# Optimization experiments

Measured on AMD Instinct MI355X. Metric: run time of the kernel, lower is better.

## Reference

```python
import jax, jax.numpy as jnp
import numpy as np

HEADS = 16
GROUPS = 4


def setup_inputs() -> dict:
    key = jax.random.key(0)
    k1, k2, k3, k4 = jax.random.split(key, 4)
    d_model = 2048
    d_kv = d_model * GROUPS // HEADS  # 512
    x = jax.random.normal(k1, (2, 2048, d_model), dtype=jnp.float32)
    Wq = jax.random.normal(k2, (d_model, d_model), dtype=jnp.float32) * (d_model ** -0.5)
    Wk = jax.random.normal(k3, (d_kv, d_model), dtype=jnp.float32) * (d_model ** -0.5)
    Wv = jax.random.normal(k4, (d_kv, d_model), dtype=jnp.float32) * (d_model ** -0.5)
    return {"x": x, "Wq": Wq, "Wk": Wk, "Wv": Wv}


def reference(x, Wq, Wk, Wv):
    b, t, c = x.shape
    hd = c // HEADS  # head dim
    h2g = HEADS // GROUPS  # query heads per kv group
    # projections (nn.Linear applies x @ W.T)
    q = (x @ Wq.T).reshape(b, t, HEADS, hd).transpose(0, 2, 1, 3)   # [b,H,t,hd]
    k = (x @ Wk.T).reshape(b, t, GROUPS, hd).transpose(0, 2, 1, 3)  # [b,G,t,hd]
    v = (x @ Wv.T).reshape(b, t, GROUPS, hd).transpose(0, 2, 1, 3)  # [b,G,t,hd]
    # GQA broadcast: group query heads by kv group
    qg = q.reshape(b, GROUPS, h2g, t, hd)                            # [b,G,h2g,t,hd]
    scores = jnp.einsum('bghqd,bgkd->bghqk', qg, k) * (hd ** -0.5)  # [b,G,h2g,t,t]
    causal = jnp.tril(jnp.ones((t, t), dtype=bool))
    scores = jnp.where(causal, scores, -jnp.inf)
    weights = jax.nn.softmax(scores, axis=-1)
    out = jnp.einsum('bghqk,bgkd->bghqd', weights, v)               # [b,G,h2g,t,hd]
    out = out.reshape(b, HEADS, t, hd).transpose(0, 2, 1, 3).reshape(b, t, c)
    return out
```

## Files before the change

kernel.cpp:

```cpp
#include <hip/hip_runtime.h>
#include <hip/hip_bf16.h>

typedef __bf16 bf16x8 __attribute__((ext_vector_type(8)));
typedef float f32x4 __attribute__((ext_vector_type(4)));

#define MFMA16(a,b,c) __builtin_amdgcn_mfma_f32_16x16x32_bf16(a,b,c,0,0,0)
#define GLL16(src, dst) __builtin_amdgcn_global_load_lds( \
    (const __attribute__((address_space(1))) unsigned int*)(src), \
    (__attribute__((address_space(3))) unsigned int*)(dst), 16, 0, 0)
#define WAIT_VM(n)  asm volatile("s_waitcnt vmcnt(" #n ")")
#define BAR() __builtin_amdgcn_s_barrier()

__device__ inline unsigned int pack_bf16(float a, float b) {
    unsigned short ua = __builtin_bit_cast(unsigned short, (__bf16)a);
    unsigned short ub = __builtin_bit_cast(unsigned short, (__bf16)b);
    return ((unsigned int)ub << 16) | ua;
}
__device__ inline short bf_s(float v) {
    __bf16 b = (__bf16)v;
    return __builtin_bit_cast(short, b);
}

__global__ __launch_bounds__(256) void cvt_all(const float* __restrict__ x,
                                               const float* __restrict__ wq,
                                               const float* __restrict__ wk,
                                               const float* __restrict__ wv,
                                               __bf16* __restrict__ xb,
                                               __bf16* __restrict__ wb) {
    int bid = blockIdx.x;
    int rb = bid >> 4, ks = bid & 15;
    int t = threadIdx.x;
    int row = t & 15;
    int k8 = ks * 16 + (t >> 4);
    int k = k8 * 8;

    const float* src;
    __bf16* dptr;
    size_t tin = (size_t)(k8 >> 2) * 512 + (size_t)(k8 & 3) * 128 + row * 8;
    if (rb < 256) {
        src  = x + (size_t)(rb * 16 + row) * 2048 + k;
        dptr = xb + (size_t)rb * 32768 + tin;
    } else {
        int wr = (rb - 256) * 16 + row;
        if (wr < 2048)      src = wq + (size_t)wr * 2048 + k;
        else if (wr < 2560) src = wk + (size_t)(wr - 2048) * 2048 + k;
        else                src = wv + (size_t)(wr - 2560) * 2048 + k;
        dptr = wb + (size_t)(rb - 256) * 32768 + tin;
    }
    float4 a = *(const float4*)src;
    float4 b = *(const float4*)(src + 4);
    bf16x8 r;
    r[0] = (__bf16)a.x; r[1] = (__bf16)a.y; r[2] = (__bf16)a.z; r[3] = (__bf16)a.w;
    r[4] = (__bf16)b.x; r[5] = (__bf16)b.y; r[6] = (__bf16)b.z; r[7] = (__bf16)b.w;
    *(bf16x8*)dptr = r;
}

__global__ __launch_bounds__(512, 6) void gemm_qkv(const __bf16* __restrict__ A,
                                                   const __bf16* __restrict__ B,
                                                   __bf16* __restrict__ Qb,
                                                   __bf16* __restrict__ Kf,
                                                   __bf16* __restrict__ Vf,
                                                   float qscale) {
    __shared__ __bf16 As[2 * 4096];
    __shared__ __bf16 Bs[2 * 4096];

    int tid = threadIdx.x;
    int wave = tid >> 6, lane = tid & 63;
    int quad = lane >> 4, l16 = lane & 15;
    int wr = wave >> 1, wc = wave & 1;

    int tm = blockIdx.x & 31, tn = blockIdx.x >> 5;

    const __bf16* Atile = A + (size_t)(tm * 8 + wave) * 32768 + lane * 8;
    const __bf16* Btile = B + (size_t)(tn * 8 + wave) * 32768 + lane * 8;

    f32x4 acc[2][4] = {};

    auto stage = [&](int kb, int buf) {
        GLL16(Atile + (size_t)kb * 512, As + buf * 4096 + wave * 512 + lane * 8);
        GLL16(Btile + (size_t)kb * 512, Bs + buf * 4096 + wave * 512 + lane * 8);
    };

    const int nk = 64;
    stage(0, 0);
    for (int it = 0; it < nk; ++it) {
        __syncthreads();
        if (it + 1 < nk) stage(it + 1, (it + 1) & 1);
        const __bf16* Ab = As + (it & 1) * 4096;
        const __bf16* Bb = Bs + (it & 1) * 4096;
        bf16x8 af[2], bfr[4];
#pragma unroll
        for (int m = 0; m < 2; ++m)
            af[m] = *(const bf16x8*)(Ab + (wr * 2 + m) * 512 + lane * 8);
#pragma unroll
        for (int n = 0; n < 4; ++n)
            bfr[n] = *(const bf16x8*)(Bb + (wc * 4 + n) * 512 + lane * 8);
#pragma unroll
        for (int m = 0; m < 2; ++m)
#pragma unroll
            for (int n = 0; n < 4; ++n)
                acc[m][n] = MFMA16(af[m], bfr[n], acc[m][n]);
    }

#pragma unroll
    for (int m = 0; m < 2; ++m) {
        int row0 = tm * 128 + wr * 32 + m * 16 + quad * 4;
        int bb = row0 >> 11, tok0 = row0 & 2047;
#pragma unroll
        for (int n = 0; n < 4; ++n) {
            int col = tn * 128 + wc * 64 + n * 16 + l16;
            if (tn < 16) {
#pragma unroll
                for (int r = 0; r < 4; ++r)
                    Qb[(size_t)(row0 + r) * 2048 + col] = (__bf16)(acc[m][n][r] * qscale);
            } else if (tn < 20) {
                int d_all = col - 2048;
                int g = d_all >> 7, dd = d_all & 127;
                int dt = dd >> 5, q4 = (dd >> 3) & 3, jj = dd & 7;
                int tb = tok0 >> 4, tl0 = tok0 & 15;
                __bf16* base = Kf + ((((size_t)(bb * 4 + g) * 128 + tb) * 4 + dt) * 512)
                               + (q4 * 16 + tl0) * 8 + jj;
#pragma unroll
                for (int r = 0; r < 4; ++r)
                    base[r * 8] = (__bf16)acc[m][n][r];
            } else {
                int d_all = col - 2560;
                int g = d_all >> 7, dd = d_all & 127;
                int nto = dd >> 4, dl = dd & 15;
                int ch = tok0 >> 6, kk = (tok0 >> 5) & 1;
                int q4v = (tok0 >> 3) & 3, jv0 = tok0 & 7;
                size_t off = ((((size_t)(bb * 4 + g) * 32 + ch) * 16) + nto * 2 + kk) * 512
                             + (q4v * 16 + dl) * 8 + jv0;
                short4 pk;
                pk.x = bf_s(acc[m][n][0]); pk.y = bf_s(acc[m][n][1]);
                pk.z = bf_s(acc[m][n][2]); pk.w = bf_s(acc[m][n][3]);
                *(short4*)(Vf + off) = pk;
            }
        }
    }
}

__global__ __launch_bounds__(256) void attn_mfma(const __bf16* __restrict__ Q,
                                                 const __bf16* __restrict__ Kf,
                                                 const __bf16* __restrict__ Vf,
                                                 float* __restrict__ O) {
    const int T = 2048, CM = 2048, HD = 128;
    __shared__ __bf16 Ks[2 * 8192];
    __shared__ __bf16 Vs[2 * 8192];
    __shared__ __bf16 Pl[8192];

    int tid = threadIdx.x;
    int wave = tid >> 6, lane = tid & 63;
    int quad = lane >> 4, l16 = lane & 15;

    int bg = blockIdx.x & 7;
    int slot = blockIdx.x >> 3;
    int qb = (slot < 32) ? (63 - slot) : (slot - 32);
    int b = bg >> 2, g = bg & 3;
    int h = g * 4 + wave;
    int q0 = qb * 32;

    bf16x8 qf[2][4];
    const __bf16* qbase = Q + (size_t)b * T * CM + (size_t)h * HD;
#pragma unroll
    for (int nt = 0; nt < 2; ++nt)
#pragma unroll
        for (int dt = 0; dt < 4; ++dt)
            qf[nt][dt] = *(const bf16x8*)(qbase + (size_t)(q0 + nt * 16 + l16) * CM
                                          + dt * 32 + quad * 8);

    const __bf16* kcb = Kf + (size_t)(b * 4 + g) * 262144;
    const __bf16* vcb = Vf + (size_t)(b * 4 + g) * 262144;

    float m_r[2] = {-1e30f, -1e30f}, l_r[2] = {0.f, 0.f};
    f32x4 o_acc[2][8] = {};
    __bf16* Pw = Pl + wave * 2048;

    auto stage_kv = [&](int ch, int buf) {
        const __bf16* kg = kcb + ch * 8192 + wave * 2048 + lane * 8;
        const __bf16* vg = vcb + ch * 8192 + wave * 2048 + lane * 8;
        __bf16* kl = Ks + buf * 8192 + wave * 2048 + lane * 8;
        __bf16* vl = Vs + buf * 8192 + wave * 2048 + lane * 8;
#pragma unroll
        for (int i = 0; i < 4; ++i) GLL16(kg + i * 512, kl + i * 512);
#pragma unroll
        for (int i = 0; i < 4; ++i) GLL16(vg + i * 512, vl + i * 512);
    };

    int nch = (qb >> 1) + 1;
    stage_kv(0, 0);
    for (int ch = 0; ch < nch; ++ch) {
        BAR();
        if (ch + 1 < nch) {
            stage_kv(ch + 1, (ch + 1) & 1);
            WAIT_VM(8);
        } else {
            WAIT_VM(0);
        }
        BAR();

        const __bf16* Kb = Ks + (ch & 1) * 8192;
        const __bf16* Vb = Vs + (ch & 1) * 8192;

        f32x4 st[2][4] = {};
        __builtin_amdgcn_s_setprio(1);
#pragma unroll
        for (int t = 0; t < 4; ++t)
#pragma unroll
            for (int dt = 0; dt < 4; ++dt) {
                bf16x8 kfv = *(const bf16x8*)(Kb + (t * 4 + dt) * 512 + lane * 8);
                st[0][t] = MFMA16(kfv, qf[0][dt], st[0][t]);
                st[1][t] = MFMA16(kfv, qf[1][dt], st[1][t]);
            }
        __builtin_amdgcn_s_setprio(0);

        bool diag = (ch == nch - 1);
        float alpha[2];
#pragma unroll
        for (int nt = 0; nt < 2; ++nt) {
            if (diag) {
                int qg = q0 + nt * 16 + l16;
#pragma unroll
                for (int t = 0; t < 4; ++t)
#pragma unroll
                    for (int r = 0; r < 4; ++r)
                        if (ch * 64 + t * 16 + quad * 4 + r > qg) st[nt][t][r] = -1e30f;
            }
            float cmax = -1e30f;
#pragma unroll
            for (int t = 0; t < 4; ++t)
                cmax = fmaxf(cmax, fmaxf(fmaxf(st[nt][t][0], st[nt][t][1]),
                                         fmaxf(st[nt][t][2], st[nt][t][3])));
            cmax = fmaxf(cmax, __shfl_xor(cmax, 16));
            cmax = fmaxf(cmax, __shfl_xor(cmax, 32));
            float mnew = fmaxf(m_r[nt], cmax);
            alpha[nt] = __expf(m_r[nt] - mnew);
            m_r[nt] = mnew;
            float ps = 0.f;
#pragma unroll
            for (int t = 0; t < 4; ++t) {
                float p0 = __expf(st[nt][t][0] - mnew);
                float p1 = __expf(st[nt][t][1] - mnew);
                float p2 = __expf(st[nt][t][2] - mnew);
                float p3 = __expf(st[nt][t][3] - mnew);
                ps += (p0 + p1) + (p2 + p3);
                int off = (nt * 2 + (t >> 1)) * 512 + ((t & 1) * 2 + (quad >> 1)) * 128
                          + l16 * 8 + (quad & 1) * 4;
                unsigned long long pk =
                    (unsigned long long)pack_bf16(p0, p1) |
                    ((unsigned long long)pack_bf16(p2, p3) << 32);
                *(unsigned long long*)(Pw + off) = pk;
            }
            ps += __shfl_xor(ps, 16);
            ps += __shfl_xor(ps, 32);
            l_r[nt] = l_r[nt] * alpha[nt] + ps;
        }

#pragma unroll
        for (int mt = 0; mt < 2; ++mt)
#pragma unroll
            for (int r = 0; r < 4; ++r) {
                float alr = __shfl(alpha[mt], quad * 4 + r);
#pragma unroll
                for (int nto = 0; nto < 8; ++nto)
                    o_acc[mt][nto][r] *= alr;
            }

        __builtin_amdgcn_s_setprio(1);
#pragma unroll
        for (int mt = 0; mt < 2; ++mt)
#pragma unroll
            for (int kk = 0; kk < 2; ++kk) {
                bf16x8 pf = *(const bf16x8*)(Pw + (mt * 2 + kk) * 512 + lane * 8);
#pragma unroll
                for (int nto = 0; nto < 8; ++nto) {
                    bf16x8 vf = *(const bf16x8*)(Vb + (nto * 2 + kk) * 512 + lane * 8);
                    o_acc[mt][nto] = MFMA16(pf, vf, o_acc[mt][nto]);
                }
            }
        __builtin_amdgcn_s_setprio(0);
    }

    float* obase = O + (size_t)b * T * CM + (size_t)h * HD;
#pragma unroll
    for (int mt = 0; mt < 2; ++mt) {
        float invl = 1.f / l_r[mt];
#pragma unroll
        for (int r = 0; r < 4; ++r) {
            float ir = __shfl(invl, quad * 4 + r);
            float* orow = obase + (size_t)(q0 + 16 * mt + quad * 4 + r) * CM;
#pragma unroll
            for (int nto = 0; nto < 8; ++nto)
                orow[nto * 16 + l16] = o_acc[mt][nto][r] * ir;
        }
    }
}

extern "C" void kernel_launch(void* const* d_in, const int* in_sizes, int n_in,
                              void* d_out, int out_size, void* d_ws, size_t ws_size,
                              hipStream_t stream) {
    const float* x  = (const float*)d_in[0];
    const float* Wq = (const float*)d_in[1];
    const float* Wk = (const float*)d_in[2];
    const float* Wv = (const float*)d_in[3];
    float* out = (float*)d_out;

    const float qscale = 0.08838834764831845f;

    __bf16* xb = (__bf16*)d_ws;
    __bf16* Wb = xb + 8388608;
    __bf16* Qb = Wb + 6291456;
    __bf16* Kfr = Qb + 8388608;
    __bf16* Vfr = Kfr + 2097152;

    cvt_all<<<7168, 256, 0, stream>>>(x, Wq, Wk, Wv, xb, Wb);
    gemm_qkv<<<768, 512, 0, stream>>>(xb, Wb, Qb, Kfr, Vfr, qscale);
    attn_mfma<<<512, 256, 0, stream>>>(Qb, Kfr, Vfr, out);
}
```

Baseline: 231.2 us.

## Load V fragments directly to registers, use exp2 softmax, skip unit rescale

V chunks are no longer staged through shared memory. Each wave loads its V fragments from global memory straight into registers at the start of each chunk, which halves LDS use and the async copy traffic. The softmax now uses exp2f, with log2(e) folded into the Q scale, and the output-accumulator rescale is skipped when every alpha in the wave equals one. The trade-off is that every wave redundantly loads the full V chunk from global or L2 with more register pressure, and global-load latency is exposed inside the loop with no prefetch.

Result: slower. 285.2 us (+23.4%).

```diff
diff --git a/kernel.cpp b/kernel.cpp
--- a/kernel.cpp
+++ b/kernel.cpp
@@ -146,7 +146,6 @@
                                                  float* __restrict__ O) {
     const int T = 2048, CM = 2048, HD = 128;
     __shared__ __bf16 Ks[2 * 8192];
-    __shared__ __bf16 Vs[2 * 8192];
     __shared__ __bf16 Pl[8192];
 
     int tid = threadIdx.x;
@@ -176,31 +175,34 @@
     f32x4 o_acc[2][8] = {};
     __bf16* Pw = Pl + wave * 2048;
 
-    auto stage_kv = [&](int ch, int buf) {
+    auto stage_k = [&](int ch, int buf) {
         const __bf16* kg = kcb + ch * 8192 + wave * 2048 + lane * 8;
-        const __bf16* vg = vcb + ch * 8192 + wave * 2048 + lane * 8;
         __bf16* kl = Ks + buf * 8192 + wave * 2048 + lane * 8;
-        __bf16* vl = Vs + buf * 8192 + wave * 2048 + lane * 8;
 #pragma unroll
         for (int i = 0; i < 4; ++i) GLL16(kg + i * 512, kl + i * 512);
-#pragma unroll
-        for (int i = 0; i < 4; ++i) GLL16(vg + i * 512, vl + i * 512);
     };
 
     int nch = (qb >> 1) + 1;
-    stage_kv(0, 0);
+    stage_k(0, 0);
     for (int ch = 0; ch < nch; ++ch) {
         BAR();
         if (ch + 1 < nch) {
-            stage_kv(ch + 1, (ch + 1) & 1);
-            WAIT_VM(8);
+            stage_k(ch + 1, (ch + 1) & 1);
+            WAIT_VM(4);
         } else {
             WAIT_VM(0);
         }
         BAR();
 
         const __bf16* Kb = Ks + (ch & 1) * 8192;
-        const __bf16* Vb = Vs + (ch & 1) * 8192;
+
+        const __bf16* vchunk = vcb + (size_t)ch * 8192 + lane * 8;
+        bf16x8 vreg[2][8];
+#pragma unroll
+        for (int kk = 0; kk < 2; ++kk)
+#pragma unroll
+            for (int nto = 0; nto < 8; ++nto)
+                vreg[kk][nto] = *(const bf16x8*)(vchunk + (nto * 2 + kk) * 512);
 
         f32x4 st[2][4] = {};
         __builtin_amdgcn_s_setprio(1);
@@ -234,15 +236,15 @@
             cmax = fmaxf(cmax, __shfl_xor(cmax, 16));
             cmax = fmaxf(cmax, __shfl_xor(cmax, 32));
             float mnew = fmaxf(m_r[nt], cmax);
-            alpha[nt] = __expf(m_r[nt] - mnew);
+            alpha[nt] = exp2f(m_r[nt] - mnew);
             m_r[nt] = mnew;
             float ps = 0.f;
 #pragma unroll
             for (int t = 0; t < 4; ++t) {
-                float p0 = __expf(st[nt][t][0] - mnew);
-                float p1 = __expf(st[nt][t][1] - mnew);
-                float p2 = __expf(st[nt][t][2] - mnew);
-                float p3 = __expf(st[nt][t][3] - mnew);
+                float p0 = exp2f(st[nt][t][0] - mnew);
+                float p1 = exp2f(st[nt][t][1] - mnew);
+                float p2 = exp2f(st[nt][t][2] - mnew);
+                float p3 = exp2f(st[nt][t][3] - mnew);
                 ps += (p0 + p1) + (p2 + p3);
                 int off = (nt * 2 + (t >> 1)) * 512 + ((t & 1) * 2 + (quad >> 1)) * 128
                           + l16 * 8 + (quad & 1) * 4;
@@ -256,15 +258,17 @@
             l_r[nt] = l_r[nt] * alpha[nt] + ps;
         }
 
-#pragma unroll
-        for (int mt = 0; mt < 2; ++mt)
-#pragma unroll
-            for (int r = 0; r < 4; ++r) {
-                float alr = __shfl(alpha[mt], quad * 4 + r);
-#pragma unroll
-                for (int nto = 0; nto < 8; ++nto)
-                    o_acc[mt][nto][r] *= alr;
-            }
+        if (!(__all(alpha[0] == 1.0f) && __all(alpha[1] == 1.0f))) {
+#pragma unroll
+            for (int mt = 0; mt < 2; ++mt)
+#pragma unroll
+                for (int r = 0; r < 4; ++r) {
+                    float alr = __shfl(alpha[mt], quad * 4 + r);
+#pragma unroll
+                    for (int nto = 0; nto < 8; ++nto)
+                        o_acc[mt][nto][r] *= alr;
+                }
+        }
 
         __builtin_amdgcn_s_setprio(1);
 #pragma unroll
@@ -273,10 +277,8 @@
             for (int kk = 0; kk < 2; ++kk) {
                 bf16x8 pf = *(const bf16x8*)(Pw + (mt * 2 + kk) * 512 + lane * 8);
 #pragma unroll
-                for (int nto = 0; nto < 8; ++nto) {
-                    bf16x8 vf = *(const bf16x8*)(Vb + (nto * 2 + kk) * 512 + lane * 8);
-                    o_acc[mt][nto] = MFMA16(pf, vf, o_acc[mt][nto]);
-                }
+                for (int nto = 0; nto < 8; ++nto)
+                    o_acc[mt][nto] = MFMA16(pf, vreg[kk][nto], o_acc[mt][nto]);
             }
         __builtin_amdgcn_s_setprio(0);
     }
@@ -305,7 +307,7 @@
     const float* Wv = (const float*)d_in[3];
     float* out = (float*)d_out;
 
-    const float qscale = 0.08838834764831845f;
+    const float qscale = 0.12751744488264393f;
 
     __bf16* xb = (__bf16*)d_ws;
     __bf16* Wb = xb + 8388608;
```
